# Kernel optimization log

Measured on AMD Instinct MI355X. Metric: run time of the kernel, lower is better.

Reference implementation:

```python
import jax, jax.numpy as jnp
import numpy as np

# Open-boundary PEPS grid: X rows (xnodes), Y cols (ynodes); boundary bond legs have size 1.
# Node axis order: (p, [o], u, r, d, l); the center node (CX, CY) carries the F_OUT leg 'o'.
# NOTE on faithfulness: in the original layer every intermediate normalization is a scalar
# per-sample rescaling, and the final result is divided by its own norm, so the layer computes
# exactly full_contraction / ||full_contraction|| per sample. Any exact contraction order with
# interleaved scalar renormalizations yields the identical function (and identical gradients).
X = Y = 4
D = 6          # bond_dim
F_IN = 2       # features_in (physical leg)
F_OUT = 10     # features_out (output leg, hard-coded to 10 in the original reshape)
CX, CY = X // 2, Y // 2
B = 1024       # batch


def _unit(t, axes):
    return t / jnp.sqrt(jnp.sum(t * t, axis=axes, keepdims=True))


def setup_inputs():
    key = jax.random.key(0)
    ki, kp, kc = jax.random.split(key, 3)
    inputs = jax.random.normal(ki, (B, X, Y, F_IN), dtype=jnp.float32)
    peps = jax.random.uniform(kp, (X, Y, F_IN, D, D, D, D), dtype=jnp.float32,
                              minval=-0.01, maxval=0.01)
    peps_center = jax.random.uniform(kc, (F_IN, F_OUT, D, D, D, D), dtype=jnp.float32,
                                     minval=-0.01, maxval=0.01)
    return {"inputs": inputs, "peps": peps, "peps_center": peps_center}


def _node(inputs, peps, peps_center, i, j):
    # contract the physical leg with the input feature vector, then normalize per sample
    center = (i, j) == (CX, CY)
    T = peps_center if center else peps[i, j]      # (p,[o],u,r,d,l)
    off = 1 if center else 0
    if i == 0:
        T = jax.lax.slice_in_dim(T, 0, 1, axis=1 + off)   # u -> size 1 (open boundary)
    if j == Y - 1:
        T = jax.lax.slice_in_dim(T, 0, 1, axis=2 + off)   # r -> size 1
    if i == X - 1:
        T = jax.lax.slice_in_dim(T, 0, 1, axis=3 + off)   # d -> size 1
    if j == 0:
        T = jax.lax.slice_in_dim(T, 0, 1, axis=4 + off)   # l -> size 1
    x = inputs[:, i, j]                                   # (B, p)
    if center:
        n = jnp.einsum('bp,pourdl->bourdl', x, T)
        return _unit(n, (1, 2, 3, 4, 5))
    n = jnp.einsum('bp,purdl->burdl', x, T)
    return _unit(n, (1, 2, 3, 4))


def _forward(inputs, peps, peps_center):
    nodes = [[_node(inputs, peps, peps_center, i, j) for j in range(Y)]
             for i in range(X)]
    ax_all = tuple(range(1, Y + 1))

    # ---- top environment: absorb rows 0 .. CX-1 -> env_top (b, d0..d{Y-1}) ----
    env = jnp.swapaxes(nodes[0][0][:, 0, :, :, 0], 1, 2)          # (b, d0, r)
    for j in range(1, Y):
        env = jnp.einsum('b...x,brdx->b...dr', env, nodes[0][j][:, 0])
    env = _unit(env[..., 0], ax_all)
    for i in range(1, CX):
        S = env[..., None]                                        # (b, u0..u{Y-1}, 1)
        for j in range(Y):
            S = jnp.einsum('bu...x,burdx->b...dr', S, nodes[i][j])
        env = _unit(S[..., 0], ax_all)
    env_top = env

    # ---- bottom environment: absorb rows X-1 .. CX+1 -> env_bot (b, u0..u{Y-1}) ----
    env = nodes[X - 1][0][:, :, :, 0, 0]                          # (b, u0, r)
    for j in range(1, Y):
        env = jnp.einsum('b...x,burx->b...ur', env,
                         nodes[X - 1][j][:, :, :, 0, :])
    env = _unit(env[..., 0], ax_all)
    for i in range(X - 2, CX, -1):
        S = env[..., None]                                        # (b, d0..d{Y-1}, 1)
        for j in range(Y):
            S = jnp.einsum('bd...x,burdx->b...ur', S, nodes[i][j])
        env = _unit(S[..., 0], ax_all)
    env_bot = env

    # ---- center row: carries the F_OUT leg 'o' ----
    S = env_top[..., None]                                        # (b, u0..u{Y-1}, 1)
    for j in range(Y):
        if j == CY:
            S = jnp.einsum('bu...x,bourdx->b...dor', S, nodes[CX][j])
        else:
            S = jnp.einsum('bu...x,burdx->b...dr', S, nodes[CX][j])
    # axes: (b, d0..d{CY}, o, d{CY+1}..d{Y-1}) -> move o last
    S = jnp.moveaxis(S[..., 0], 2 + CY, -1)                       # (b, d0..d{Y-1}, o)
    out = jnp.einsum('bwxyzo,bwxyz->bo', S, env_bot)              # Y == 4
    return out / jnp.linalg.norm(out, axis=1, keepdims=True)


def reference(inputs, peps, peps_center):
    return _forward(inputs, peps, peps_center)
```

## Files before the change

kernel.cpp:

```cpp
#include <hip/hip_runtime.h>
#include <math.h>

#define BLK 512

typedef __attribute__((ext_vector_type(8))) short s16x8;
typedef __attribute__((ext_vector_type(16))) float f32x16;
typedef __attribute__((ext_vector_type(4))) unsigned short u16x4;

__device__ __forceinline__ float b2f(unsigned short h) {
    union { unsigned u; float f; } x; x.u = ((unsigned)h) << 16; return x.f;
}
__device__ __forceinline__ unsigned short f2b(float f) {
    union { float f; unsigned u; } x; x.f = f;
    unsigned r = x.u + 0x7fffu + ((x.u >> 16) & 1u);
    return (unsigned short)(r >> 16);
}

#define SITE(i, j) (peps + (size_t)((i) * 4 + (j)) * 2 * 1296)


#define MFMA_PHASE(NKB, NNT, TB, TSTR) do {                                    \
    if (wid < 7) {                                                             \
        int m0 = (wid == 6) ? 184 : wid*32;                                    \
        _Pragma("unroll") for (int kb = 0; kb < NKB; ++kb) {                   \
            s16x8 _av = *(const s16x8*)&Ebuf[(m0 + col)*56 + kb*16 + q*8];     \
            _Pragma("unroll") for (int nt = 0; nt < NNT; ++nt) {               \
                s16x8 _bf = *(const s16x8*)&(TB)[(nt*4 + col)*(TSTR) + kb*16 + q*8]; \
                acc[nt] = __builtin_amdgcn_mfma_f32_32x32x16_bf16(             \
                    _av, _bf, acc[nt], 0, 0, 0);                               \
            } } } } while (0)

#define SCAT(NNT, MTAB, NOFFE) do {                                            \
    if (wid < 7) {                                                             \
        int mbase = ((wid == 6) ? 184 : wid*32) + 4*q;                         \
        int noffv[2]; bool okv[2];                                             \
        _Pragma("unroll") for (int nt = 0; nt < NNT; ++nt) {                   \
            int n = nt*4 + col;                                                \
            noffv[nt] = (NOFFE);                                               \
            okv[nt]   = (nt == 0) || (n >= 32);                                \
        }                                                                      \
        _Pragma("unroll") for (int rr = 0; rr < 4; ++rr) {                     \
            if (wid == 6 && rr == 0) continue;                                 \
            u16x4 mt4 = *(const u16x4*)&(MTAB)[mbase + 8*rr];                  \
            _Pragma("unroll") for (int nt = 0; nt < NNT; ++nt) {               \
                _Pragma("unroll") for (int jp = 0; jp < 2; ++jp) {             \
                    unsigned pk;                                               \
                    float _lo = acc[nt][rr*4 + jp*2];                          \
                    float _hi = acc[nt][rr*4 + jp*2 + 1];                      \
                    asm("v_cvt_pk_bf16_f32 %0, %1, %2"                         \
                        : "=v"(pk) : "v"(_lo), "v"(_hi));                      \
                    if (okv[nt]) {                                             \
                        *(unsigned short*)((char*)Ebuf + (int)mt4[jp*2]   + noffv[nt]) = (unsigned short)pk;         \
                        *(unsigned short*)((char*)Ebuf + (int)mt4[jp*2+1] + noffv[nt]) = (unsigned short)(pk >> 16); \
                    } } } } } } while (0)

#define SCAT_D() do {                                                          \
    if (wid < 7) {                                                             \
        int mbase = ((wid == 6) ? 184 : wid*32) + 4*q;                         \
        bool ok = (col < 6);                                                   \
        int noff = col * 112;                                                  \
        _Pragma("unroll") for (int rr = 0; rr < 4; ++rr) {                     \
            if (wid == 6 && rr == 0) continue;                                 \
            u16x4 mt4 = *(const u16x4*)&mtabD[mbase + 8*rr];                   \
            _Pragma("unroll") for (int jp = 0; jp < 2; ++jp) {                 \
                unsigned pk;                                                   \
                float _lo = acc[0][rr*4 + jp*2];                               \
                float _hi = acc[0][rr*4 + jp*2 + 1];                           \
                asm("v_cvt_pk_bf16_f32 %0, %1, %2"                             \
                    : "=v"(pk) : "v"(_lo), "v"(_hi));                          \
                if (ok) {                                                      \
                    *(unsigned short*)((char*)Ebuf + (int)mt4[jp*2]   + noff) = (unsigned short)pk;         \
                    *(unsigned short*)((char*)Ebuf + (int)mt4[jp*2+1] + noff) = (unsigned short)(pk >> 16); \
                } } } } } while (0)

#define SCATTER(NNT, NLIM, PUT) do {                                           \
    unsigned short* EbS = Ebuf;                                                \
    float* T1S = (float*)Ebuf; (void)EbS; (void)T1S;                           \
    if (wid < 7) {                                                             \
        int m0 = (wid == 6) ? 184 : wid*32;                                    \
        _Pragma("unroll") for (int nt = 0; nt < NNT; ++nt) {                   \
            int n = nt*4 + col;                                                \
            if ((NNT == 2 && nt == 1 && n < 32) || n >= NLIM) continue;        \
            _Pragma("unroll") for (int r = 0; r < 16; ++r) {                   \
                int m = m0 + (r&3) + 8*(r>>2) + 4*q;                           \
                if (wid == 6 && m < 192) continue;                             \
                float v = acc[nt][r];                                          \
                PUT;                                                           \
            } } } } while (0)

#define ACC0() do {                                                            \
    _Pragma("unroll") for (int nt = 0; nt < 2; ++nt)                           \
    _Pragma("unroll") for (int r = 0; r < 16; ++r) acc[nt][r] = 0.f;           \
    } while (0)

__global__ __launch_bounds__(BLK, 8)
void peps_fused(const float* __restrict__ inputs,
                const float* __restrict__ peps,
                const float* __restrict__ pepsc,
                float* __restrict__ out)
{
    __shared__ __align__(16) unsigned short Ebuf[216 * 56];
    __shared__ __align__(16) unsigned short TA[36 * 56];
    __shared__ __align__(16) unsigned short TBt[36 * 56];
    __shared__ __align__(16) unsigned short Tk6[2 * 36 * 16];
    __shared__ __align__(16) float CTf[936];
    __shared__ __align__(8) unsigned short mtabA[216];
    __shared__ __align__(8) unsigned short mtabB[216];
    __shared__ __align__(8) unsigned short mtabC[216];
    __shared__ __align__(8) unsigned short mtabD[216];
    __shared__ float xs[32];
    __shared__ float red[96];

    const int b0  = blockIdx.x;
    const int tid = threadIdx.x;
    const int lid = tid & 63;
    const int q   = lid >> 5;
    const int col = lid & 31;
    const int wid = __builtin_amdgcn_readfirstlane(tid >> 6);

    f32x16 acc[2];

    {
        uint4* ez = (uint4*)&Ebuf[0];
        const uint4 z = make_uint4(0u, 0u, 0u, 0u);
        for (int i2 = tid; i2 < 1512; i2 += BLK) ez[i2] = z;
        if (tid < 32) xs[tid] = inputs[b0 * 32 + tid] * 100.0f;
        if (tid < 216) {
            int m = tid;
            mtabA[m] = (unsigned short)(((m%36)*336 + (m/36)*6) * 2);
            mtabB[m] = (unsigned short)(((m/6)*336 + (m%6)*6) * 2);
            mtabC[m] = (unsigned short)(((m/36)*2016 + (m%6)*336 + ((m/6)%6)*6) * 2);
            mtabD[m] = (unsigned short)(((m%36)*336 + (m/36)) * 2);
        }
    }
    __syncthreads();

    for (int idx = tid; idx < 216; idx += BLK) {
        int x = idx/36, d = (idx/6)%6, r = idx%6;
        int g0 = x + d*6 + r*36, g3 = x + d*216 + r*36;
        float a, c;
        a = SITE(0,1)[g0]; c = SITE(0,1)[g0+1296];
        CTf[idx]       = xs[2]  * a + xs[3]  * c;
        a = SITE(0,2)[g0]; c = SITE(0,2)[g0+1296];
        CTf[216 + idx] = xs[4]  * a + xs[5]  * c;
        a = SITE(3,1)[g3]; c = SITE(3,1)[g3+1296];
        CTf[432 + idx] = xs[26] * a + xs[27] * c;
        a = SITE(3,2)[g3]; c = SITE(3,2)[g3+1296];
        CTf[648 + idx] = xs[28] * a + xs[29] * c;
    }
    for (int idx = tid; idx < 36; idx += BLK) {
        int x = idx/6, d = idx%6;
        float a, c;
        a = SITE(0,3)[x + d*6];   c = SITE(0,3)[x + d*6 + 1296];
        CTf[864 + idx] = xs[6]  * a + xs[7]  * c;
        a = SITE(3,3)[x + d*216]; c = SITE(3,3)[x + d*216 + 1296];
        CTf[900 + idx] = xs[30] * a + xs[31] * c;
        int u = x, r = d;
        float a0 = SITE(0,0)[r*36 + u*6],   c0 = SITE(0,0)[r*36 + u*6 + 1296];
        float a3 = SITE(3,0)[u*216 + r*36], c3 = SITE(3,0)[u*216 + r*36 + 1296];
        Ebuf[u*56 + 6  + r] = f2b(xs[0]  * a0 + xs[1]  * c0);
        Ebuf[u*56 + 18 + r] = f2b(xs[24] * a3 + xs[25] * c3);
    }
    {
        const float *s10 = SITE(1,0), *s20 = SITE(2,0);
        for (int idx = tid; idx < 576; idx += BLK) {
            int n = idx/16, k = idx%16;
            float v00 = 0.f, v10 = 0.f;
            if (k < 6) {
                int g = k*216 + (n/6)*6 + (n%6)*36;
                float a = s10[g], c = s10[g+1296];
                v00 = xs[8]  * a + xs[9]  * c;
                a = s20[g]; c = s20[g+1296];
                v10 = xs[16] * a + xs[17] * c;
            }
            Tk6[n*16 + k]       = f2b(v00);
            Tk6[576 + n*16 + k] = f2b(v10);
        }
    }
    {
        const float* s = SITE(1,1);
        for (int idx = tid; idx < 1728; idx += BLK) {
            int n = idx/48, k = idx%48;
            float v0 = 0.f;
            if (k < 36) {
                int g = (k/6)*216 + (k%6) + (n/6)*6 + (n%6)*36;
                float a = s[g], c = s[g+1296];
                v0 = xs[10] * a + xs[11] * c;
            }
            TA[n*56 + k] = f2b(v0);
        }
    }
    for (int idx = tid; idx < 432; idx += BLK) {
        int n = idx/12, k = 36 + idx%12;
        TBt[n*56 + k] = 0;
    }
    __syncthreads();

    for (int t2 = tid; t2 < 216; t2 += BLK) {
        int m = t2/36, n = t2%36;
        float a0 = 0.f, a3 = 0.f;
        #pragma unroll
        for (int k = 0; k < 6; ++k) {
            a0 = fmaf(b2f(Ebuf[m*56 + 6  + k]), CTf[k*36 + n],       a0);
            a3 = fmaf(b2f(Ebuf[m*56 + 18 + k]), CTf[432 + k*36 + n], a3);
        }
        int o = (m*6 + n/6)*56 + n%6;
        Ebuf[o + 12] = f2b(a0);
        Ebuf[o + 24] = f2b(a3);
    }
    __syncthreads();

    for (int t2 = tid; t2 < 1296; t2 += BLK) {
        int m = t2/36, n = t2%36;
        float a0 = 0.f, a3 = 0.f;
        #pragma unroll
        for (int k = 0; k < 6; ++k) {
            a0 = fmaf(b2f(Ebuf[m*56 + 12 + k]), CTf[216 + k*36 + n], a0);
            a3 = fmaf(b2f(Ebuf[m*56 + 24 + k]), CTf[648 + k*36 + n], a3);
        }
        int o = (m*6 + n/6)*56 + n%6;
        Ebuf[o + 6]  = f2b(a0);
        Ebuf[o + 18] = f2b(a3);
    }
    __syncthreads();

    for (int t2 = tid; t2 < 1296; t2 += BLK) {
        int m = t2/6, n = t2%6;
        float a0 = 0.f, a3 = 0.f;
        #pragma unroll
        for (int k = 0; k < 6; ++k) {
            a0 = fmaf(b2f(Ebuf[m*56 + 6  + k]), CTf[864 + k*6 + n], a0);
            a3 = fmaf(b2f(Ebuf[m*56 + 18 + k]), CTf[900 + k*6 + n], a3);
        }
        Ebuf[((m % 36)*6 + n)*56 + m/36] = f2b(a0);
        TBt[((m % 6)*6 + n)*56 + m/6]    = f2b(a3);
    }
    __syncthreads();

    ACC0();
    MFMA_PHASE(1, 2, Tk6, 16);
    __syncthreads();
    SCAT(2, mtabA, ((n/6)*56 + n%6)*2);
    {
        const float* s = SITE(1,3);
        for (int idx = tid; idx < 288; idx += BLK) {
            int n = idx/48, k = idx%48;
            float v0 = 0.f;
            if (k < 36) {
                int g = (k/6)*216 + (k%6) + n*6;
                float a = s[g], c = s[g+1296];
                v0 = xs[14] * a + xs[15] * c;
            }
            ((unsigned short*)CTf)[n*56 + k] = f2b(v0);
        }
    }
    __syncthreads();
    ACC0();
    MFMA_PHASE(3, 2, TA, 56);
    __syncthreads();
    SCAT(2, mtabA, ((n/6)*56 + n%6)*2);
    {
        const float* s = SITE(1,2);
        for (int idx = tid; idx < 1728; idx += BLK) {
            int n = idx/48, k = idx%48;
            float v0 = 0.f;
            if (k < 36) {
                int g = (k/6)*216 + (k%6) + (n/6)*6 + (n%6)*36;
                float a = s[g], c = s[g+1296];
                v0 = xs[12] * a + xs[13] * c;
            }
            TA[n*56 + k] = f2b(v0);
        }
    }
    __syncthreads();
    ACC0();
    MFMA_PHASE(3, 2, TA, 56);
    __syncthreads();
    SCAT(2, mtabA, ((n/6)*56 + n%6)*2);
    {
        const float* s = SITE(2,1);
        for (int idx = tid; idx < 1728; idx += BLK) {
            int n = idx/48, k = idx%48;
            float v0 = 0.f;
            if (k < 36) {
                int g = (k/6)*216 + (k%6) + (n/6)*6 + (n%6)*36;
                float a = s[g], c = s[g+1296];
                v0 = xs[18] * a + xs[19] * c;
            }
            TA[n*56 + k] = f2b(v0);
        }
    }
    __syncthreads();
    ACC0();
    MFMA_PHASE(3, 1, (unsigned short*)CTf, 56);
    __syncthreads();
    SCAT_D();
    {
        const float* s = SITE(2,3);
        for (int idx = tid; idx < 288; idx += BLK) {
            int n = idx/48, k = idx%48;
            float v0 = 0.f;
            if (k < 36) {
                int g = (k/6)*216 + (k%6)*6 + n;
                float a = s[g], c = s[g+1296];
                v0 = xs[22] * a + xs[23] * c;
            }
            ((unsigned short*)CTf)[n*56 + k] = f2b(v0);
        }
    }
    __syncthreads();

    ACC0();
    MFMA_PHASE(1, 2, (Tk6 + 576), 16);
    __syncthreads();
    SCAT(2, mtabA, ((n/6)*56 + n%6)*2);
    __syncthreads();
    ACC0();
    MFMA_PHASE(3, 2, TA, 56);
    __syncthreads();
    SCAT(2, mtabB, ((n%6)*56 + n/6)*2);
    __syncthreads();
    ACC0();
    MFMA_PHASE(3, 2, TBt, 56);
    __syncthreads();
    SCAT(2, mtabC, ((n/6)*56 + n%6)*2);
    __syncthreads();
    ACC0();
    MFMA_PHASE(3, 1, (unsigned short*)CTf, 56);
    __syncthreads();
    SCATTER(1, 6, T1S[m*6 + n] = v);
    __syncthreads();

    float part[10];
    #pragma unroll
    for (int o = 0; o < 10; ++o) part[o] = 0.f;
    {
        const float* T1p = (const float*)Ebuf;
        for (int c = tid; c < 1296; c += BLK) {
            int u2 = c / 216, r2 = (c / 36) % 6, d2 = (c / 6) % 6, r1 = c % 6;
            int e6 = u2*216 + r1*36 + d2*6 + r2;
            float t1 = T1p[e6];
            #pragma unroll
            for (int o = 0; o < 10; ++o) {
                float c0 = pepsc[o * 1296 + c];
                float c1 = pepsc[(10 + o) * 1296 + c];
                part[o] = fmaf(t1, xs[20] * c0 + xs[21] * c1, part[o]);
            }
        }
    }
    #pragma unroll
    for (int off = 32; off >= 1; off >>= 1)
        #pragma unroll
        for (int o = 0; o < 10; ++o)
            part[o] += __shfl_down(part[o], off, 64);
    if (lid == 0) {
        #pragma unroll
        for (int o = 0; o < 10; ++o) red[wid * 10 + o] = part[o];
    }
    __syncthreads();
    if (tid < 10) {
        float s = 0.f;
        #pragma unroll
        for (int w = 0; w < 8; ++w) s += red[w * 10 + tid];
        red[80 + tid] = s;
    }
    __syncthreads();
    if (tid == 0) {
        float n2 = 0.f;
        #pragma unroll
        for (int o = 0; o < 10; ++o) n2 += red[80 + o] * red[80 + o];
        red[90] = 1.0f / sqrtf(n2);
    }
    __syncthreads();
    if (tid < 10) out[b0 * 10 + tid] = red[80 + tid] * red[90];
}

extern "C" void kernel_launch(void* const* d_in, const int* in_sizes, int n_in,
                              void* d_out, int out_size, void* d_ws, size_t ws_size,
                              hipStream_t stream) {
    const float* inputs = (const float*)d_in[0];
    const float* peps   = (const float*)d_in[1];
    const float* pepsc  = (const float*)d_in[2];
    float* outp = (float*)d_out;
    const int B = in_sizes[0] / 32;
    peps_fused<<<dim3(B), dim3(BLK), 0, stream>>>(inputs, peps, pepsc, outp);
}
```

Measured before the change: 94.61 us.

## Add prep kernel to pre-gather PEPS weights into contiguous interleaved workspace layout

A new prep kernel gathers the strided PEPS site tensors into a contiguous workspace in exactly the order each per-sample build stage consumes. Each element is stored as an (a,c) float2 pair for the two physical components, zero-padded to the MFMA tile strides, and the center tensor is permuted so the final reduction reads it linearly. The main kernel then loads these with coalesced float4 reads and packs pairs to bf16 with a single conversion instruction, replacing scattered gathers and per-element index math. This adds a second kernel launch and a workspace pass on every call. It is recomputed each call from the weights only.

```diff
diff --git a/kernel.cpp b/kernel.cpp
--- a/kernel.cpp
+++ b/kernel.cpp
@@ -17,6 +17,65 @@
 }
 
 #define SITE(i, j) (peps + (size_t)((i) * 4 + (j)) * 2 * 1296)
+
+__global__ __launch_bounds__(256)
+void peps_prep(const float* __restrict__ peps, const float* __restrict__ pepsc,
+               float* __restrict__ ws)
+{
+    int idx = blockIdx.x * 256 + threadIdx.x;
+    float2* W = (float2*)ws;
+    float* PC = ws + 2 * 8880;
+    if (idx < 8880) {
+        const float* s = peps;
+        int g = -1;
+        if (idx < 6048) {
+            int seg = idx / 2016, i = idx - seg * 2016;
+            int n = i / 56, k = i % 56;
+            s = (seg == 0) ? SITE(1,1) : (seg == 1) ? SITE(1,2) : SITE(2,1);
+            if (k < 36) g = (k/6)*216 + (k%6) + (n/6)*6 + (n%6)*36;
+        } else if (idx < 6384) {
+            int i = idx - 6048, n = i / 56, k = i % 56;
+            s = SITE(1,3);
+            if (k < 36) g = (k/6)*216 + (k%6) + n*6;
+        } else if (idx < 6720) {
+            int i = idx - 6384, n = i / 56, k = i % 56;
+            s = SITE(2,3);
+            if (k < 36) g = (k/6)*216 + (k%6)*6 + n;
+        } else if (idx < 7872) {
+            int i = idx - 6720; int w2 = i / 576; i -= w2 * 576;
+            int n = i / 16, k = i % 16;
+            s = w2 ? SITE(2,0) : SITE(1,0);
+            if (k < 6) g = k*216 + (n/6)*6 + (n%6)*36;
+        } else if (idx < 8808) {
+            int i = idx - 7872;
+            if (i < 864) {
+                int seg = i / 216, j = i - seg * 216;
+                int x = j/36, d = (j/6)%6, r = j%6;
+                if (seg == 0)      { s = SITE(0,1); g = x + d*6   + r*36; }
+                else if (seg == 1) { s = SITE(0,2); g = x + d*6   + r*36; }
+                else if (seg == 2) { s = SITE(3,1); g = x + d*216 + r*36; }
+                else               { s = SITE(3,2); g = x + d*216 + r*36; }
+            } else {
+                int j = i - 864, seg = j / 36, t = j % 36;
+                int x = t/6, d = t%6;
+                if (seg == 0) { s = SITE(0,3); g = x + d*6; }
+                else          { s = SITE(3,3); g = x + d*216; }
+            }
+        } else if (idx < 8844) {
+            int i = idx - 8808; s = SITE(0,0); g = (i%6)*36 + (i/6)*6;
+        } else {
+            int i = idx - 8844; s = SITE(3,0); g = (i/6)*216 + (i%6)*36;
+        }
+        float a = 0.f, c = 0.f;
+        if (g >= 0) { a = s[g]; c = s[g + 1296]; }
+        W[idx] = make_float2(a, c);
+    } else if (idx < 8880 + 25920) {
+        int i = idx - 8880;
+        int o = i / 1296, e = i % 1296;
+        int u2 = e / 216, r1 = (e / 36) % 6, d2 = (e / 6) % 6, r2 = e % 6;
+        PC[i] = pepsc[o * 1296 + u2*216 + r2*36 + d2*6 + r1];
+    }
+}
 
 
 #define MFMA_PHASE(NKB, NNT, TB, TSTR) do {                                    \
@@ -93,10 +152,19 @@
     _Pragma("unroll") for (int r = 0; r < 16; ++r) acc[nt][r] = 0.f;           \
     } while (0)
 
+#define BUILD2(DST, SRCF2, NPAIR, X0, X1) do {                                 \
+    const float4* _w4 = (const float4*)(SRCF2);                                \
+    for (int p = tid; p < (NPAIR); p += BLK) {                                 \
+        float4 w = _w4[p];                                                     \
+        float _lo = (X0)*w.x + (X1)*w.y, _hi = (X0)*w.z + (X1)*w.w;            \
+        unsigned pk;                                                           \
+        asm("v_cvt_pk_bf16_f32 %0, %1, %2" : "=v"(pk) : "v"(_lo), "v"(_hi));   \
+        *(unsigned*)&(DST)[p*2] = pk;                                          \
+    } } while (0)
+
 __global__ __launch_bounds__(BLK, 8)
 void peps_fused(const float* __restrict__ inputs,
-                const float* __restrict__ peps,
-                const float* __restrict__ pepsc,
+                const float* __restrict__ ws,
                 float* __restrict__ out)
 {
     __shared__ __align__(16) unsigned short Ebuf[216 * 56];
@@ -118,6 +186,9 @@
     const int col = lid & 31;
     const int wid = __builtin_amdgcn_readfirstlane(tid >> 6);
 
+    const float2* W = (const float2*)ws;
+    const float*  PC = ws + 2 * 8880;
+
     f32x16 acc[2];
 
     {
@@ -135,61 +206,34 @@
     }
     __syncthreads();
 
-    for (int idx = tid; idx < 216; idx += BLK) {
-        int x = idx/36, d = (idx/6)%6, r = idx%6;
-        int g0 = x + d*6 + r*36, g3 = x + d*216 + r*36;
-        float a, c;
-        a = SITE(0,1)[g0]; c = SITE(0,1)[g0+1296];
-        CTf[idx]       = xs[2]  * a + xs[3]  * c;
-        a = SITE(0,2)[g0]; c = SITE(0,2)[g0+1296];
-        CTf[216 + idx] = xs[4]  * a + xs[5]  * c;
-        a = SITE(3,1)[g3]; c = SITE(3,1)[g3+1296];
-        CTf[432 + idx] = xs[26] * a + xs[27] * c;
-        a = SITE(3,2)[g3]; c = SITE(3,2)[g3+1296];
-        CTf[648 + idx] = xs[28] * a + xs[29] * c;
-    }
-    for (int idx = tid; idx < 36; idx += BLK) {
-        int x = idx/6, d = idx%6;
-        float a, c;
-        a = SITE(0,3)[x + d*6];   c = SITE(0,3)[x + d*6 + 1296];
-        CTf[864 + idx] = xs[6]  * a + xs[7]  * c;
-        a = SITE(3,3)[x + d*216]; c = SITE(3,3)[x + d*216 + 1296];
-        CTf[900 + idx] = xs[30] * a + xs[31] * c;
-        int u = x, r = d;
-        float a0 = SITE(0,0)[r*36 + u*6],   c0 = SITE(0,0)[r*36 + u*6 + 1296];
-        float a3 = SITE(3,0)[u*216 + r*36], c3 = SITE(3,0)[u*216 + r*36 + 1296];
-        Ebuf[u*56 + 6  + r] = f2b(xs[0]  * a0 + xs[1]  * c0);
-        Ebuf[u*56 + 18 + r] = f2b(xs[24] * a3 + xs[25] * c3);
+    for (int idx = tid; idx < 936; idx += BLK) {
+        float2 w = W[7872 + idx];
+        int ci = (idx < 216) ? 2 : (idx < 432) ? 4 : (idx < 648) ? 26
+               : (idx < 864) ? 28 : (idx < 900) ? 6 : 30;
+        CTf[idx] = xs[ci] * w.x + xs[ci + 1] * w.y;
+    }
+    if (tid < 36) {
+        float2 w0 = W[8808 + tid], w3 = W[8844 + tid];
+        int u = tid / 6, r = tid % 6;
+        Ebuf[u*56 + 6  + r] = f2b(xs[0]  * w0.x + xs[1]  * w0.y);
+        Ebuf[u*56 + 18 + r] = f2b(xs[24] * w3.x + xs[25] * w3.y);
     }
     {
-        const float *s10 = SITE(1,0), *s20 = SITE(2,0);
-        for (int idx = tid; idx < 576; idx += BLK) {
-            int n = idx/16, k = idx%16;
-            float v00 = 0.f, v10 = 0.f;
-            if (k < 6) {
-                int g = k*216 + (n/6)*6 + (n%6)*36;
-                float a = s10[g], c = s10[g+1296];
-                v00 = xs[8]  * a + xs[9]  * c;
-                a = s20[g]; c = s20[g+1296];
-                v10 = xs[16] * a + xs[17] * c;
-            }
-            Tk6[n*16 + k]       = f2b(v00);
-            Tk6[576 + n*16 + k] = f2b(v10);
-        }
-    }
-    {
-        const float* s = SITE(1,1);
-        for (int idx = tid; idx < 1728; idx += BLK) {
-            int n = idx/48, k = idx%48;
-            float v0 = 0.f;
-            if (k < 36) {
-                int g = (k/6)*216 + (k%6) + (n/6)*6 + (n%6)*36;
-                float a = s[g], c = s[g+1296];
-                v0 = xs[10] * a + xs[11] * c;
-            }
-            TA[n*56 + k] = f2b(v0);
-        }
-    }
+        const float4* W10 = (const float4*)(W + 6720);
+        const float4* W20 = (const float4*)(W + 7296);
+        for (int p = tid; p < 288; p += BLK) {
+            float4 w = W10[p];
+            float lo = xs[8]*w.x + xs[9]*w.y, hi = xs[8]*w.z + xs[9]*w.w;
+            unsigned pk;
+            asm("v_cvt_pk_bf16_f32 %0, %1, %2" : "=v"(pk) : "v"(lo), "v"(hi));
+            *(unsigned*)&Tk6[p*2] = pk;
+            w = W20[p];
+            lo = xs[16]*w.x + xs[17]*w.y; hi = xs[16]*w.z + xs[17]*w.w;
+            asm("v_cvt_pk_bf16_f32 %0, %1, %2" : "=v"(pk) : "v"(lo), "v"(hi));
+            *(unsigned*)&Tk6[576 + p*2] = pk;
+        }
+    }
+    BUILD2(TA, W + 0, 1008, xs[10], xs[11]);
     for (int idx = tid; idx < 432; idx += BLK) {
         int n = idx/12, k = 36 + idx%12;
         TBt[n*56 + k] = 0;
@@ -241,73 +285,25 @@
     MFMA_PHASE(1, 2, Tk6, 16);
     __syncthreads();
     SCAT(2, mtabA, ((n/6)*56 + n%6)*2);
-    {
-        const float* s = SITE(1,3);
-        for (int idx = tid; idx < 288; idx += BLK) {
-            int n = idx/48, k = idx%48;
-            float v0 = 0.f;
-            if (k < 36) {
-                int g = (k/6)*216 + (k%6) + n*6;
-                float a = s[g], c = s[g+1296];
-                v0 = xs[14] * a + xs[15] * c;
-            }
-            ((unsigned short*)CTf)[n*56 + k] = f2b(v0);
-        }
-    }
+    BUILD2((unsigned short*)CTf, W + 6048, 168, xs[14], xs[15]);
     __syncthreads();
     ACC0();
     MFMA_PHASE(3, 2, TA, 56);
     __syncthreads();
     SCAT(2, mtabA, ((n/6)*56 + n%6)*2);
-    {
-        const float* s = SITE(1,2);
-        for (int idx = tid; idx < 1728; idx += BLK) {
-            int n = idx/48, k = idx%48;
-            float v0 = 0.f;
-            if (k < 36) {
-                int g = (k/6)*216 + (k%6) + (n/6)*6 + (n%6)*36;
-                float a = s[g], c = s[g+1296];
-                v0 = xs[12] * a + xs[13] * c;
-            }
-            TA[n*56 + k] = f2b(v0);
-        }
-    }
+    BUILD2(TA, W + 2016, 1008, xs[12], xs[13]);
     __syncthreads();
     ACC0();
     MFMA_PHASE(3, 2, TA, 56);
     __syncthreads();
     SCAT(2, mtabA, ((n/6)*56 + n%6)*2);
-    {
-        const float* s = SITE(2,1);
-        for (int idx = tid; idx < 1728; idx += BLK) {
-            int n = idx/48, k = idx%48;
-            float v0 = 0.f;
-            if (k < 36) {
-                int g = (k/6)*216 + (k%6) + (n/6)*6 + (n%6)*36;
-                float a = s[g], c = s[g+1296];
-                v0 = xs[18] * a + xs[19] * c;
-            }
-            TA[n*56 + k] = f2b(v0);
-        }
-    }
+    BUILD2(TA, W + 4032, 1008, xs[18], xs[19]);
     __syncthreads();
     ACC0();
     MFMA_PHASE(3, 1, (unsigned short*)CTf, 56);
     __syncthreads();
     SCAT_D();
-    {
-        const float* s = SITE(2,3);
-        for (int idx = tid; idx < 288; idx += BLK) {
-            int n = idx/48, k = idx%48;
-            float v0 = 0.f;
-            if (k < 36) {
-                int g = (k/6)*216 + (k%6)*6 + n;
-                float a = s[g], c = s[g+1296];
-                v0 = xs[22] * a + xs[23] * c;
-            }
-            ((unsigned short*)CTf)[n*56 + k] = f2b(v0);
-        }
-    }
+    BUILD2((unsigned short*)CTf, W + 6384, 168, xs[22], xs[23]);
     __syncthreads();
 
     ACC0();
@@ -336,14 +332,12 @@
     for (int o = 0; o < 10; ++o) part[o] = 0.f;
     {
         const float* T1p = (const float*)Ebuf;
-        for (int c = tid; c < 1296; c += BLK) {
-            int u2 = c / 216, r2 = (c / 36) % 6, d2 = (c / 6) % 6, r1 = c % 6;
-            int e6 = u2*216 + r1*36 + d2*6 + r2;
-            float t1 = T1p[e6];
+        for (int e = tid; e < 1296; e += BLK) {
+            float t1 = T1p[e];
             #pragma unroll
             for (int o = 0; o < 10; ++o) {
-                float c0 = pepsc[o * 1296 + c];
-                float c1 = pepsc[(10 + o) * 1296 + c];
+                float c0 = PC[o * 1296 + e];
+                float c1 = PC[(10 + o) * 1296 + e];
                 part[o] = fmaf(t1, xs[20] * c0 + xs[21] * c1, part[o]);
             }
         }
@@ -382,6 +376,8 @@
     const float* peps   = (const float*)d_in[1];
     const float* pepsc  = (const float*)d_in[2];
     float* outp = (float*)d_out;
+    float* ws   = (float*)d_ws;
     const int B = in_sizes[0] / 32;
-    peps_fused<<<dim3(B), dim3(BLK), 0, stream>>>(inputs, peps, pepsc, outp);
-}
+    peps_prep<<<dim3(136), dim3(256), 0, stream>>>(peps, pepsc, ws);
+    peps_fused<<<dim3(B), dim3(BLK), 0, stream>>>(inputs, ws, outp);
+}
```

Result: faster. 92.02 us (-2.7%).
